# Optimization experiments

Measured on AMD Instinct MI355X. Metric: run time of the kernel, lower is better.

## Reference

```python
import jax, jax.numpy as jnp
import numpy as np

B = 4096
D = 1024
N = 9000000
TEMPERATURE = 0.1
GAMMA = 0.8
ALPHA = 0.5
EPS = 1e-14


def setup_inputs() -> dict:
    key = jax.random.key(0)
    k1, k2, k3, k4, k5 = jax.random.split(key, 5)
    zis = jax.random.normal(k1, (B, D), dtype=jnp.float32)
    zjs = jax.random.normal(k2, (B, D), dtype=jnp.float32)
    s_I = jax.random.uniform(k3, (N,), dtype=jnp.float32)
    s_T = jax.random.uniform(k4, (N,), dtype=jnp.float32)
    b_I = jnp.zeros((N,), dtype=jnp.float32)
    b_T = jnp.zeros((N,), dtype=jnp.float32)
    ids = jax.random.randint(k5, (B,), 0, N, dtype=jnp.int64 if jax.config.jax_enable_x64 else jnp.int32)
    return {"zis": zis, "zjs": zjs, "s_I": s_I, "s_T": s_T, "b_I": b_I, "b_T": b_T, "ids": ids}


def reference(zis, zjs, s_I, s_T, b_I, b_T, ids):
    sg = jax.lax.stop_gradient
    # L2 normalize embeddings (norm=True path)
    zis = zis / jnp.linalg.norm(zis, axis=1, keepdims=True)
    zjs = zjs / jnp.linalg.norm(zjs, axis=1, keepdims=True)
    sim = jnp.einsum('id,jd->ij', zis, zjs)            # [B, B]
    diag = jnp.diagonal(sim)                            # [B]
    image_diffs = sim - diag[:, None]
    text_diffs = sim - diag[None, :]
    # detached, temperature-scaled diffs (torch .clone().detach_())
    idd = sg(image_diffs) / TEMPERATURE
    tdd = sg(text_diffs) / TEMPERATURE
    # online max tracking (per-id running max b)
    old_b_I = b_I[ids]                                  # gather [B]
    new_b_I = jnp.maximum(idd.max(axis=1), old_b_I)
    old_b_T = b_T[ids]
    new_b_T = jnp.maximum(tdd.max(axis=0), old_b_T)
    mask_neg = 1.0 - jnp.eye(B, dtype=sim.dtype)
    exp_image_diffs = jnp.exp(idd - new_b_I[:, None]) * mask_neg
    exp_text_diffs = jnp.exp(tdd - new_b_T[None, :]) * mask_neg
    g_I = exp_image_diffs.sum(axis=1) / (B - 1)         # [B]
    g_T = exp_text_diffs.sum(axis=0) / (B - 1)          # [B]
    # EMA of softmax denominator with rescaling for new max
    s_I_new = (1.0 - GAMMA) * s_I[ids] * jnp.exp(old_b_I - new_b_I) + GAMMA * g_I
    s_T_new = (1.0 - GAMMA) * s_T[ids] * jnp.exp(old_b_T - new_b_T) + GAMMA * g_T
    # state writes (side effects in torch; computed for fidelity)
    b_I = b_I.at[ids].set(new_b_I)
    b_T = b_T.at[ids].set(new_b_T)
    s_I = s_I.at[ids].set(s_I_new)
    s_T = s_T.at[ids].set(s_T_new)
    s_I_c = jnp.maximum(s_I_new, EPS)
    s_T_c = jnp.maximum(s_T_new, EPS)
    weights_image = exp_image_diffs / s_I_c[:, None]    # detached weights
    weights_text = exp_text_diffs / s_T_c[None, :]
    image_loss = (weights_image * image_diffs).sum(axis=1) / (B - 1)
    text_loss = (weights_text * text_diffs).sum(axis=0) / (B - 1)
    total_loss = ALPHA * image_loss.mean() + (1.0 - ALPHA) * text_loss.mean()
    return total_loss
```

## Files before the change

kernel.cpp:

```cpp
#include <hip/hip_runtime.h>
#include <stdint.h>

#define B_ 4096
#define D_ 1024
#define NT 16
#define TINV 10.0f
#define LOG2E 1.4426950408889634f
#define KE (TINV * LOG2E)
#define INV_BM1 (1.0f / 4095.0f)

typedef __bf16 bf16x8 __attribute__((ext_vector_type(8)));
typedef float f32x4 __attribute__((ext_vector_type(4)));

__device__ __forceinline__ unsigned short f2bf(float x) {
  uint32_t b = __float_as_uint(x);
  b += 0x7FFF + ((b >> 16) & 1);
  return (unsigned short)(b >> 16);
}
__device__ __forceinline__ float bf2f(unsigned short u) {
  return __uint_as_float(((uint32_t)u) << 16);
}

__device__ __forceinline__ void gload16(const void* g, void* l) {
  __builtin_amdgcn_global_load_lds(
      (const __attribute__((address_space(1))) uint32_t*)g,
      (__attribute__((address_space(3))) uint32_t*)l, 16, 0, 0);
}

__global__ __launch_bounds__(256) void k_normalize(const float* __restrict__ zis,
                                                   const float* __restrict__ zjs,
                                                   unsigned short* __restrict__ Abf,
                                                   unsigned short* __restrict__ Bbf) {
  int r = blockIdx.x;
  const float* src;
  unsigned short* dst;
  if (r < B_) { src = zis + (size_t)r * D_; dst = Abf + (size_t)r * D_; }
  else        { src = zjs + (size_t)(r - B_) * D_; dst = Bbf + (size_t)(r - B_) * D_; }
  int t = threadIdx.x;
  float4 v = reinterpret_cast<const float4*>(src)[t];
  float ss = v.x*v.x + v.y*v.y + v.z*v.z + v.w*v.w;
  #pragma unroll
  for (int o = 32; o >= 1; o >>= 1) ss += __shfl_down(ss, o);
  __shared__ float red[4];
  if ((t & 63) == 0) red[t >> 6] = ss;
  __syncthreads();
  float sc = rsqrtf(red[0] + red[1] + red[2] + red[3]);
  ushort4 o4;
  o4.x = f2bf(v.x * sc); o4.y = f2bf(v.y * sc);
  o4.z = f2bf(v.z * sc); o4.w = f2bf(v.w * sc);
  reinterpret_cast<ushort4*>(dst)[t] = o4;
}

#define LDA(MH)                                                              \
  { _Pragma("unroll") for (int m4_ = 0; m4_ < 4; ++m4_) {                    \
      const unsigned short* p_ = &Abase[((MH)*64 + m4_*16 + fr) * 64];       \
      a[m4_][0] = *reinterpret_cast<const bf16x8*>(&p_[ce0]);                \
      a[m4_][1] = *reinterpret_cast<const bf16x8*>(&p_[ce1]); } }

#define LDB(NH)                                                              \
  { _Pragma("unroll") for (int n2_ = 0; n2_ < 2; ++n2_) {                    \
      const unsigned short* p_ = &Bbase[(bn_off + ((NH)*2+n2_)*16 + fr) * 64]; \
      b[(NH)*2+n2_][0] = *reinterpret_cast<const bf16x8*>(&p_[ce0]);         \
      b[(NH)*2+n2_][1] = *reinterpret_cast<const bf16x8*>(&p_[ce1]); } }

#define MFMAQ(MH, NH)                                                        \
  { _Pragma("unroll") for (int m4_ = 0; m4_ < 4; ++m4_) {                    \
      _Pragma("unroll") for (int n2_ = 0; n2_ < 2; ++n2_) {                  \
        acc[(MH)*4+m4_][(NH)*2+n2_] = __builtin_amdgcn_mfma_f32_16x16x32_bf16( \
            a[m4_][0], b[(NH)*2+n2_][0], acc[(MH)*4+m4_][(NH)*2+n2_], 0,0,0);  \
        acc[(MH)*4+m4_][(NH)*2+n2_] = __builtin_amdgcn_mfma_f32_16x16x32_bf16( \
            a[m4_][1], b[(NH)*2+n2_][1], acc[(MH)*4+m4_][(NH)*2+n2_], 0,0,0); } } }

#define STAGE_A(T, H)                                                        \
  { const unsigned short* g_ = Ag + (size_t)((H)*128)*D_ + (T)*64;           \
    gload16(g_ + so0, &lds[(T)&1][0][H][q0*512]);                            \
    gload16(g_ + so1, &lds[(T)&1][0][H][q1*512]); }

#define STAGE_B(T, H)                                                        \
  { const unsigned short* g_ = Bg + (size_t)((H)*128)*D_ + (T)*64;           \
    gload16(g_ + so0, &lds[(T)&1][1][H][q0*512]);                            \
    gload16(g_ + so1, &lds[(T)&1][1][H][q1*512]); }

#define SYNC_PRE                                                             \
  __builtin_amdgcn_s_barrier();                                              \
  asm volatile("s_waitcnt lgkmcnt(0)" ::: "memory");                         \
  __builtin_amdgcn_sched_barrier(0);                                         \
  __builtin_amdgcn_s_setprio(1);

#define SYNC_POST                                                            \
  __builtin_amdgcn_s_setprio(0);                                             \
  __builtin_amdgcn_sched_barrier(0);                                         \
  __builtin_amdgcn_s_barrier();

__global__ __launch_bounds__(512, 2) void k_gemm(const unsigned short* __restrict__ A,
                                                 const unsigned short* __restrict__ B,
                                                 unsigned short* __restrict__ C,
                                                 float* __restrict__ diagp) {
  __shared__ unsigned short lds[2][2][2][8192];
  const int tid = threadIdx.x;
  const int wid = tid >> 6;
  const int lane = tid & 63;
  const int wm = wid >> 2;
  const int wn = wid & 3;
  const int bRow = blockIdx.y * 256;
  const int bCol = blockIdx.x * 256;
  const unsigned short* Ag = A + (size_t)bRow * D_;
  const unsigned short* Bg = B + (size_t)bCol * D_;

  const int q0 = wid * 2, q1 = q0 + 1;
  const int srow = q0 * 8 + (lane >> 3);
  const int scol = ((lane & 7) * 8) ^ (((lane >> 5) & 1) << 4);
  const size_t so0 = (size_t)srow * D_ + scol;
  const size_t so1 = (size_t)(srow + 8) * D_ + (scol ^ 32);

  const int fr = lane & 15;
  const int sx = (((lane >> 2) & 1) << 4) | (((lane >> 3) & 1) << 5);
  const int ce0 = ((lane >> 4) * 8) ^ sx;
  const int ce1 = (((lane >> 4) * 8) + 32) ^ sx;
  const int bn_off = (wn & 1) * 64;

  f32x4 acc[8][4] = {};

  STAGE_A(0, 0); STAGE_A(0, 1); STAGE_B(0, 0); STAGE_B(0, 1);
  STAGE_B(1, 0); STAGE_A(1, 0);
  asm volatile("s_waitcnt vmcnt(4)" ::: "memory");
  __builtin_amdgcn_sched_barrier(0);
  __builtin_amdgcn_s_barrier();

  for (int t = 0; t < NT; ++t) {
    const int s = t & 1;
    const unsigned short* Abase = &lds[s][0][wm][0];
    const unsigned short* Bbase = &lds[s][1][wn >> 1][0];
    bf16x8 a[4][2], b[4][2];

    LDA(0); LDB(0);
    if (t + 1 < NT) { STAGE_B(t + 1, 1); }
    SYNC_PRE; MFMAQ(0, 0); SYNC_POST;

    LDB(1);
    if (t + 1 < NT) { STAGE_A(t + 1, 1); }
    SYNC_PRE; MFMAQ(0, 1); SYNC_POST;

    LDA(1);
    if (t + 2 < NT) { __builtin_amdgcn_sched_barrier(0); STAGE_B(t + 2, 0); }
    SYNC_PRE; MFMAQ(1, 0); SYNC_POST;

    if (t + 2 < NT) { __builtin_amdgcn_sched_barrier(0); STAGE_A(t + 2, 0); }
    __builtin_amdgcn_s_setprio(1);
    MFMAQ(1, 1);
    __builtin_amdgcn_s_setprio(0);
    if (t < NT - 2) {
      asm volatile("s_waitcnt vmcnt(4)" ::: "memory");
    } else if (t == NT - 2) {
      asm volatile("s_waitcnt vmcnt(0)" ::: "memory");
    }
    __builtin_amdgcn_sched_barrier(0);
    if (t < NT - 1) __builtin_amdgcn_s_barrier();
  }

  const int fr4 = (lane >> 4) * 4;
  #pragma unroll
  for (int m = 0; m < 8; ++m)
    #pragma unroll
    for (int n = 0; n < 4; ++n)
      #pragma unroll
      for (int q = 0; q < 4; ++q) {
        float v = acc[m][n][q];
        int rg = bRow + wm * 128 + m * 16 + fr4 + q;
        int cg = bCol + wn * 64 + n * 16 + fr;
        if (rg == cg) diagp[rg] = v;
        float p = __shfl_xor(v, 1);
        if (!(lane & 1)) {
          uint32_t u = (uint32_t)f2bf(v) | ((uint32_t)f2bf(p) << 16);
          *reinterpret_cast<uint32_t*>(&C[(size_t)rg * B_ + cg]) = u;
        }
      }
}

__global__ __launch_bounds__(256) void k_fused(const unsigned short* __restrict__ sim,
    const float* __restrict__ diag,
    const float* __restrict__ bI, const float* __restrict__ sI,
    const int* __restrict__ ids,
    float* __restrict__ LI, float* __restrict__ cmax_p,
    float* __restrict__ cE_p, float* __restrict__ cE2_p) {
  const int i0 = blockIdx.x * 16;
  const int t = threadIdx.x;
  const int w = t >> 6, lane = t & 63;
  __shared__ float rowPart[16][4][3];

  float cmax[16], cE[16], cE2[16];
  #pragma unroll
  for (int k = 0; k < 16; ++k) { cmax[k] = -3.4e38f; cE[k] = 0.f; cE2[k] = 0.f; }

  for (int r = 0; r < 16; ++r) {
    const unsigned short* sp = sim + (size_t)(i0 + r) * B_ + t * 16;
    uint4 u0 = *reinterpret_cast<const uint4*>(sp);
    uint4 u1 = *reinterpret_cast<const uint4*>(sp + 8);
    float x[16];
    x[0]  = __uint_as_float(u0.x << 16); x[1]  = __uint_as_float(u0.x & 0xffff0000u);
    x[2]  = __uint_as_float(u0.y << 16); x[3]  = __uint_as_float(u0.y & 0xffff0000u);
    x[4]  = __uint_as_float(u0.z << 16); x[5]  = __uint_as_float(u0.z & 0xffff0000u);
    x[6]  = __uint_as_float(u0.w << 16); x[7]  = __uint_as_float(u0.w & 0xffff0000u);
    x[8]  = __uint_as_float(u1.x << 16); x[9]  = __uint_as_float(u1.x & 0xffff0000u);
    x[10] = __uint_as_float(u1.y << 16); x[11] = __uint_as_float(u1.y & 0xffff0000u);
    x[12] = __uint_as_float(u1.z << 16); x[13] = __uint_as_float(u1.z & 0xffff0000u);
    x[14] = __uint_as_float(u1.w << 16); x[15] = __uint_as_float(u1.w & 0xffff0000u);
    float rmx = -3.4e38f, rE = 0.f, rE2 = 0.f;
    #pragma unroll
    for (int k = 0; k < 16; ++k) {
      float e = exp2f(x[k] * KE);
      rmx = fmaxf(rmx, x[k]);
      rE += e;
      rE2 = fmaf(e, x[k], rE2);
      cmax[k] = fmaxf(cmax[k], x[k]);
      cE[k] += e;
      cE2[k] = fmaf(e, x[k], cE2[k]);
    }
    #pragma unroll
    for (int o = 32; o >= 1; o >>= 1) {
      rmx = fmaxf(rmx, __shfl_down(rmx, o));
      rE += __shfl_down(rE, o);
      rE2 += __shfl_down(rE2, o);
    }
    if (lane == 0) { rowPart[r][w][0] = rmx; rowPart[r][w][1] = rE; rowPart[r][w][2] = rE2; }
  }
  __syncthreads();
  if (t < 16) {
    int i = i0 + t;
    float mx = fmaxf(fmaxf(rowPart[t][0][0], rowPart[t][1][0]),
                     fmaxf(rowPart[t][2][0], rowPart[t][3][0]));
    float E  = (rowPart[t][0][1] + rowPart[t][1][1]) + (rowPart[t][2][1] + rowPart[t][3][1]);
    float E2 = (rowPart[t][0][2] + rowPart[t][1][2]) + (rowPart[t][2][2] + rowPart[t][3][2]);
    float dg = diag[i];
    float ed = exp2f(dg * KE);
    int id = ids[i];
    float oldb = bI[id];
    float newb = fmaxf((mx - dg) * TINV, oldb);
    float sc = exp2f(-(dg * TINV + newb) * LOG2E);
    float S1 = (E - ed) * sc;
    float S2 = (E2 - dg * E) * sc;
    float g = S1 * INV_BM1;
    float sn = 0.2f * sI[id] * exp2f((oldb - newb) * LOG2E) + 0.8f * g;
    LI[i] = S2 / fmaxf(sn, 1e-14f) * INV_BM1;
  }
  size_t base = (size_t)blockIdx.x * B_ + t * 16;
  #pragma unroll
  for (int k = 0; k < 16; ++k) {
    cmax_p[base + k] = cmax[k];
    cE_p[base + k]   = cE[k];
    cE2_p[base + k]  = cE2[k];
  }
}

__global__ __launch_bounds__(256) void k_colred(
    const float* __restrict__ diag,
    const float* __restrict__ cmax_p, const float* __restrict__ cE_p,
    const float* __restrict__ cE2_p,
    const float* __restrict__ bT, const float* __restrict__ sT,
    const int* __restrict__ ids, const float* __restrict__ LI,
    float* __restrict__ partial) {
  const int t = threadIdx.x;
  const int cidx = t >> 5;
  const int sub = t & 31;
  const int j = blockIdx.x * 8 + cidx;
  float mx = -3.4e38f, E = 0.f, E2 = 0.f;
  #pragma unroll
  for (int k = 0; k < 8; ++k) {
    size_t o = (size_t)(sub + 32 * k) * B_ + j;
    mx = fmaxf(mx, cmax_p[o]);
    E += cE_p[o];
    E2 += cE2_p[o];
  }
  #pragma unroll
  for (int o = 16; o >= 1; o >>= 1) {
    mx = fmaxf(mx, __shfl_down(mx, o, 32));
    E += __shfl_down(E, o, 32);
    E2 += __shfl_down(E2, o, 32);
  }
  __shared__ float red[8];
  if (sub == 0) {
    float dg = diag[j];
    float ed = exp2f(dg * KE);
    int id = ids[j];
    float oldb = bT[id];
    float newb = fmaxf((mx - dg) * TINV, oldb);
    float sc = exp2f(-(dg * TINV + newb) * LOG2E);
    float S1 = (E - ed) * sc;
    float S2 = (E2 - dg * E) * sc;
    float g = S1 * INV_BM1;
    float sn = 0.2f * sT[id] * exp2f((oldb - newb) * LOG2E) + 0.8f * g;
    float lt = S2 / fmaxf(sn, 1e-14f) * INV_BM1;
    red[cidx] = (0.5f * LI[j] + 0.5f * lt) * (1.0f / (float)B_);
  }
  __syncthreads();
  if (t == 0) {
    float s = 0.f;
    #pragma unroll
    for (int k = 0; k < 8; ++k) s += red[k];
    partial[blockIdx.x] = s;
  }
}

__global__ void k_final2(const float* __restrict__ partial, float* __restrict__ out) {
  int t = threadIdx.x;
  float v = partial[t];
  #pragma unroll
  for (int o = 32; o >= 1; o >>= 1) v += __shfl_down(v, o);
  __shared__ float red[8];
  if ((t & 63) == 0) red[t >> 6] = v;
  __syncthreads();
  if (t == 0) {
    float s = 0.f;
    #pragma unroll
    for (int k = 0; k < 8; ++k) s += red[k];
    out[0] = s;
  }
}

extern "C" void kernel_launch(void* const* d_in, const int* in_sizes, int n_in,
                              void* d_out, int out_size, void* d_ws, size_t ws_size,
                              hipStream_t stream) {
  const float* zis = (const float*)d_in[0];
  const float* zjs = (const float*)d_in[1];
  const float* s_I = (const float*)d_in[2];
  const float* s_T = (const float*)d_in[3];
  const float* b_I = (const float*)d_in[4];
  const float* b_T = (const float*)d_in[5];
  const int*   ids = (const int*)d_in[6];

  char* ws = (char*)d_ws;
  size_t off = 0;
  auto alloc = [&](size_t bytes) -> void* {
    void* p = ws + off;
    off = (off + bytes + 255) & ~(size_t)255;
    return p;
  };
  unsigned short* Abf = (unsigned short*)alloc((size_t)B_ * D_ * 2);
  unsigned short* Bbf = (unsigned short*)alloc((size_t)B_ * D_ * 2);
  unsigned short* sim = (unsigned short*)alloc((size_t)B_ * B_ * 2);
  float* diag   = (float*)alloc(B_ * 4);
  float* cmax_p = (float*)alloc((size_t)256 * B_ * 4);
  float* cE_p   = (float*)alloc((size_t)256 * B_ * 4);
  float* cE2_p  = (float*)alloc((size_t)256 * B_ * 4);
  float* LI     = (float*)alloc(B_ * 4);
  float* partial = (float*)alloc(512 * 4);

  k_normalize<<<2 * B_, 256, 0, stream>>>(zis, zjs, Abf, Bbf);
  k_gemm<<<dim3(16, 16), 512, 0, stream>>>(Abf, Bbf, sim, diag);
  k_fused<<<256, 256, 0, stream>>>(sim, diag, b_I, s_I, ids, LI, cmax_p, cE_p, cE2_p);
  k_colred<<<512, 256, 0, stream>>>(diag, cmax_p, cE_p, cE2_p, b_T, s_T, ids, LI, partial);
  k_final2<<<1, 512, 0, stream>>>(partial, (float*)d_out);
}
```

Baseline: 91.36 us.

## Simplify GEMM sync to single barriers and widen LDS swizzle pattern

Replaces the paired barrier, lgkmcnt wait and sched_barrier around each MFMA quadrant with one s_barrier after each quadrant, and removes the sched_barrier fences so the compiler can interleave LDS reads with MFMAs. The LDS XOR swizzle gains an extra bit on both the global-to-LDS store side and the fragment read side, to reduce bank conflicts. This cuts synchronisation overhead, but it depends on the compiler inserting the right waitcnts. Any mismatch between the new store and read swizzles would give wrong results.

Result: faster. 87.46 us (-4.3%).

```diff
diff --git a/kernel.cpp b/kernel.cpp
--- a/kernel.cpp
+++ b/kernel.cpp
@@ -80,17 +80,6 @@
   { const unsigned short* g_ = Bg + (size_t)((H)*128)*D_ + (T)*64;           \
     gload16(g_ + so0, &lds[(T)&1][1][H][q0*512]);                            \
     gload16(g_ + so1, &lds[(T)&1][1][H][q1*512]); }
-
-#define SYNC_PRE                                                             \
-  __builtin_amdgcn_s_barrier();                                              \
-  asm volatile("s_waitcnt lgkmcnt(0)" ::: "memory");                         \
-  __builtin_amdgcn_sched_barrier(0);                                         \
-  __builtin_amdgcn_s_setprio(1);
-
-#define SYNC_POST                                                            \
-  __builtin_amdgcn_s_setprio(0);                                             \
-  __builtin_amdgcn_sched_barrier(0);                                         \
-  __builtin_amdgcn_s_barrier();
 
 __global__ __launch_bounds__(512, 2) void k_gemm(const unsigned short* __restrict__ A,
                                                  const unsigned short* __restrict__ B,
@@ -109,12 +98,14 @@
 
   const int q0 = wid * 2, q1 = q0 + 1;
   const int srow = q0 * 8 + (lane >> 3);
-  const int scol = ((lane & 7) * 8) ^ (((lane >> 5) & 1) << 4);
-  const size_t so0 = (size_t)srow * D_ + scol;
-  const size_t so1 = (size_t)(srow + 8) * D_ + (scol ^ 32);
+  const int f0 = (((lane >> 4) & 1) << 3) | (((lane >> 5) & 1) << 4);
+  const int scol0 = ((lane & 7) * 8) ^ f0;
+  const size_t so0 = (size_t)srow * D_ + scol0;
+  const size_t so1 = (size_t)(srow + 8) * D_ + (scol0 ^ 32);
 
   const int fr = lane & 15;
-  const int sx = (((lane >> 2) & 1) << 4) | (((lane >> 3) & 1) << 5);
+  const int sx = (((lane >> 1) & 1) << 3) | (((lane >> 2) & 1) << 4) |
+                 (((lane >> 3) & 1) << 5);
   const int ce0 = ((lane >> 4) * 8) ^ sx;
   const int ce1 = (((lane >> 4) * 8) + 32) ^ sx;
   const int bn_off = (wn & 1) * 64;
@@ -124,7 +115,6 @@
   STAGE_A(0, 0); STAGE_A(0, 1); STAGE_B(0, 0); STAGE_B(0, 1);
   STAGE_B(1, 0); STAGE_A(1, 0);
   asm volatile("s_waitcnt vmcnt(4)" ::: "memory");
-  __builtin_amdgcn_sched_barrier(0);
   __builtin_amdgcn_s_barrier();
 
   for (int t = 0; t < NT; ++t) {
@@ -135,17 +125,26 @@
 
     LDA(0); LDB(0);
     if (t + 1 < NT) { STAGE_B(t + 1, 1); }
-    SYNC_PRE; MFMAQ(0, 0); SYNC_POST;
+    __builtin_amdgcn_s_setprio(1);
+    MFMAQ(0, 0);
+    __builtin_amdgcn_s_setprio(0);
+    __builtin_amdgcn_s_barrier();
 
     LDB(1);
     if (t + 1 < NT) { STAGE_A(t + 1, 1); }
-    SYNC_PRE; MFMAQ(0, 1); SYNC_POST;
+    __builtin_amdgcn_s_setprio(1);
+    MFMAQ(0, 1);
+    __builtin_amdgcn_s_setprio(0);
+    __builtin_amdgcn_s_barrier();
 
     LDA(1);
-    if (t + 2 < NT) { __builtin_amdgcn_sched_barrier(0); STAGE_B(t + 2, 0); }
-    SYNC_PRE; MFMAQ(1, 0); SYNC_POST;
-
-    if (t + 2 < NT) { __builtin_amdgcn_sched_barrier(0); STAGE_A(t + 2, 0); }
+    if (t + 2 < NT) { STAGE_B(t + 2, 0); }
+    __builtin_amdgcn_s_setprio(1);
+    MFMAQ(1, 0);
+    __builtin_amdgcn_s_setprio(0);
+    __builtin_amdgcn_s_barrier();
+
+    if (t + 2 < NT) { STAGE_A(t + 2, 0); }
     __builtin_amdgcn_s_setprio(1);
     MFMAQ(1, 1);
     __builtin_amdgcn_s_setprio(0);
@@ -154,7 +153,6 @@
     } else if (t == NT - 2) {
       asm volatile("s_waitcnt vmcnt(0)" ::: "memory");
     }
-    __builtin_amdgcn_sched_barrier(0);
     if (t < NT - 1) __builtin_amdgcn_s_barrier();
   }
 
```
